# Optimization experiments

Measured on AMD Instinct MI355X. Metric: run time of the kernel, lower is better.

## Reference

```python
import jax, jax.numpy as jnp
import numpy as np

N_NODES = 100000


def gcn_conv(x, src, dst, norm, W, b, n):
    # x: [N, F_in]; src/dst: [E'] (with self loops); norm: [E']
    xw = x @ W                                   # [N, F_out]
    msg = xw[src] * norm[:, None]                # [E', F_out]
    agg = jax.ops.segment_sum(msg, dst, num_segments=n)
    return agg + b


def _self_loops_and_norm(edge_index, n):
    loop = jnp.arange(n, dtype=edge_index.dtype)
    src = jnp.concatenate([edge_index[0], loop])
    dst = jnp.concatenate([edge_index[1], loop])
    deg = jax.ops.segment_sum(jnp.ones_like(dst, dtype=jnp.float32), dst, num_segments=n)
    dis = jnp.where(deg > 0, jax.lax.rsqrt(jnp.maximum(deg, 1.0)), 0.0)
    norm = dis[src] * dis[dst]
    return src, dst, norm


def setup_inputs() -> dict:
    key = jax.random.key(0)
    k1, k2, k3, k4, k5, k6 = jax.random.split(key, 6)
    n, e = N_NODES, 1600000
    f_in, f_hid, f_out = 64, 128, 64
    x = jax.random.normal(k1, (n, f_in), dtype=jnp.float32)
    edge_index = jax.random.randint(k2, (2, e), 0, n, dtype=jnp.int64)
    # Glorot init like PyG GCNConv
    W0 = jax.random.normal(k3, (f_in, f_hid), dtype=jnp.float32) * (1.0 / np.sqrt(f_in))
    b0 = jnp.zeros((f_hid,), dtype=jnp.float32)
    W1 = jax.random.normal(k4, (f_hid, f_out), dtype=jnp.float32) * (1.0 / np.sqrt(f_hid))
    b1 = jnp.zeros((f_out,), dtype=jnp.float32)
    return {"x": x, "edge_index": edge_index, "W0": W0, "b0": b0, "W1": W1, "b1": b1}


def reference(x, edge_index, W0, b0, W1, b1):
    n = x.shape[0]
    src, dst, norm = _self_loops_and_norm(edge_index, n)
    h = gcn_conv(x, src, dst, norm, W0, b0, n)
    h = jax.nn.relu(h)
    out = gcn_conv(h, src, dst, norm, W1, b1, n)
    return jax.nn.sigmoid(out)
```

## Files before the change

kernel.cpp:

```cpp
#include <hip/hip_runtime.h>
#include <hip/hip_fp16.h>
#include <math.h>


#define FIN 64
#define FHID 128
#define FOUT 64
#define NPB 128
#define LOGNPB 7
#define BMAX 800
#define G 256
#define CAP 4096

typedef _Float16 f16x2 __attribute__((ext_vector_type(2)));

#if defined(__has_builtin)
#if __has_builtin(__builtin_amdgcn_fdot2)
#define HAS_FDOT2 1
#endif
#endif

__device__ __forceinline__ float dot2(f16x2 a, f16x2 b, float c) {
#ifdef HAS_FDOT2
    return __builtin_amdgcn_fdot2(a, b, c, false);
#else
    c = fmaf((float)a[0], (float)b[0], c);
    return fmaf((float)a[1], (float)b[1], c);
#endif
}


__global__ __launch_bounds__(1024) void khist(const int* __restrict__ dst,
                                              int* __restrict__ ghist,
                                              int e, int B, int chunk) {
    __shared__ int h[BMAX];
    int g = blockIdx.x, t = threadIdx.x;
    for (int i = t; i < B; i += 1024) h[i] = 0;
    __syncthreads();
    int lo = g * chunk, hi = min(e, lo + chunk);
    for (int i = lo + t; i < hi; i += 1024)
        atomicAdd(&h[dst[i] >> LOGNPB], 1);
    __syncthreads();
    for (int i = t; i < B; i += 1024) ghist[i * G + g] = h[i];
}

__global__ __launch_bounds__(256) void kscanA(const int* __restrict__ ghist,
                                              int* __restrict__ gbase,
                                              int* __restrict__ tot, int B) {
    int b = blockIdx.x * 256 + threadIdx.x;
    if (b >= B) return;
    int run = 0;
    #pragma unroll 8
    for (int g = 0; g < G; ++g) {
        int v = ghist[b * G + g];
        gbase[b * G + g] = run;
        run += v;
    }
    tot[b] = run;
}

__global__ __launch_bounds__(256) void kscanB(const int* __restrict__ tot,
                                              int* __restrict__ bb, int B, int e) {
    __shared__ int s[256];
    __shared__ int chunkoff;
    int t = threadIdx.x;
    if (t == 0) chunkoff = 0;
    __syncthreads();
    for (int c0 = 0; c0 < B; c0 += 256) {
        int v = (c0 + t < B) ? tot[c0 + t] : 0;
        s[t] = v;
        __syncthreads();
        for (int off = 1; off < 256; off <<= 1) {
            int u = (t >= off) ? s[t - off] : 0;
            __syncthreads();
            s[t] += u;
            __syncthreads();
        }
        if (c0 + t < B) bb[c0 + t] = s[t] - v + chunkoff;
        __syncthreads();
        if (t == 255) chunkoff += s[255];
        __syncthreads();
    }
    if (t == 0) bb[B] = e;
}

__global__ __launch_bounds__(1024) void kscatter(const int* __restrict__ src,
                                                 const int* __restrict__ dst,
                                                 const int* __restrict__ gbase,
                                                 const int* __restrict__ bb,
                                                 unsigned* __restrict__ pk,
                                                 int e, int B, int chunk) {
    __shared__ int cur[BMAX];
    int g = blockIdx.x, t = threadIdx.x;
    for (int b = t; b < B; b += 1024) cur[b] = bb[b] + gbase[b * G + g];
    __syncthreads();
    int lo = g * chunk, hi = min(e, lo + chunk);
    for (int i = lo + t; i < hi; i += 1024) {
        int d = dst[i], s = src[i], b = d >> LOGNPB;
        int p = atomicAdd(&cur[b], 1);
        pk[p] = ((unsigned)(d & (NPB - 1)) << 17) | (unsigned)s;
    }
}

__global__ __launch_bounds__(256) void kpsort(const unsigned* __restrict__ pk,
                                              const int* __restrict__ bb,
                                              const float* __restrict__ x,
                                              int* __restrict__ ssrc,
                                              int* __restrict__ rp,
                                              float* __restrict__ dis,
                                              __half* __restrict__ yh,
                                              int n, int e) {
    __shared__ int cnt[NPB];
    __shared__ int pre[NPB];
    __shared__ float disl[NPB];
    __shared__ unsigned stage[CAP];
    int b = blockIdx.x, t = threadIdx.x;
    int lo = bb[b], hi = bb[b + 1], m = hi - lo;
    if (t < NPB) cnt[t] = 0;
    __syncthreads();
    for (int i = lo + t; i < hi; i += 256)
        atomicAdd(&cnt[pk[i] >> 17], 1);
    __syncthreads();
    if (t < NPB) pre[t] = cnt[t];
    __syncthreads();
    #pragma unroll
    for (int off = 1; off < NPB; off <<= 1) {
        int v = (t < NPB && t >= off) ? pre[t - off] : 0;
        __syncthreads();
        if (t < NPB) pre[t] += v;
        __syncthreads();
    }
    if (t < NPB) {
        int node = b * NPB + t;
        int c = cnt[t];
        int bs = lo + pre[t] - c;
        float dv = rsqrtf(1.0f + (float)c);
        disl[t] = dv;
        if (node < n) {
            rp[node] = bs;
            dis[node] = dv;
        }
        cnt[t] = bs - lo;
    }
    if (b == 0 && t == 0) rp[n] = e;
    __syncthreads();
    if (m <= CAP) {
        for (int i = lo + t; i < hi; i += 256) {
            unsigned v = pk[i];
            int p = atomicAdd(&cnt[v >> 17], 1);
            stage[p] = v & 0x1FFFF;
        }
        __syncthreads();
        for (int i = t; i < m; i += 256) ssrc[lo + i] = (int)stage[i];
    } else {
        for (int i = lo + t; i < hi; i += 256) {
            unsigned v = pk[i];
            int p = atomicAdd(&cnt[v >> 17], 1);
            ssrc[lo + p] = (int)(v & 0x1FFFF);
        }
    }
    for (int i = t; i < NPB * 16; i += 256) {
        int node = b * NPB + (i >> 4);
        if (node < n) {
            float d = disl[i >> 4];
            int gi = b * (NPB * 16) + i;
            float4 v = reinterpret_cast<const float4*>(x)[gi];
            __half2 h0, h1;
            h0.x = __float2half(d * v.x); h0.y = __float2half(d * v.y);
            h1.x = __float2half(d * v.z); h1.y = __float2half(d * v.w);
            reinterpret_cast<__half2*>(yh)[gi * 2 + 0] = h0;
            reinterpret_cast<__half2*>(yh)[gi * 2 + 1] = h1;
        }
    }
}

__global__ __launch_bounds__(256) void k_pull16(
        const int* __restrict__ rp, const int* __restrict__ ssrc,
        const float* __restrict__ dis, const __half* __restrict__ yh,
        const float* __restrict__ b1, float* __restrict__ outp,
        __half* __restrict__ outph, int n, int sig) {
    int node4 = blockIdx.x * 4 + (threadIdx.x >> 6);
    if (node4 >= n) return;
    int node = __builtin_amdgcn_readfirstlane(node4);
    int f = threadIdx.x & 63;
    float a0 = __half2float(yh[(size_t)node * 64 + f]);
    float a1 = 0.f, a2 = 0.f, a3 = 0.f, a4 = 0.f, a5 = 0.f, a6 = 0.f, a7 = 0.f;
    int j = rp[node], end = rp[node + 1];
    for (; j + 7 < end; j += 8) {
        int s0 = ssrc[j],     s1 = ssrc[j + 1], s2 = ssrc[j + 2], s3 = ssrc[j + 3];
        int s4 = ssrc[j + 4], s5 = ssrc[j + 5], s6 = ssrc[j + 6], s7 = ssrc[j + 7];
        a0 += __half2float(yh[(size_t)s0 * 64 + f]);
        a1 += __half2float(yh[(size_t)s1 * 64 + f]);
        a2 += __half2float(yh[(size_t)s2 * 64 + f]);
        a3 += __half2float(yh[(size_t)s3 * 64 + f]);
        a4 += __half2float(yh[(size_t)s4 * 64 + f]);
        a5 += __half2float(yh[(size_t)s5 * 64 + f]);
        a6 += __half2float(yh[(size_t)s6 * 64 + f]);
        a7 += __half2float(yh[(size_t)s7 * 64 + f]);
    }
    for (; j + 1 < end; j += 2) {
        int s0 = ssrc[j], s1 = ssrc[j + 1];
        a0 += __half2float(yh[(size_t)s0 * 64 + f]);
        a1 += __half2float(yh[(size_t)s1 * 64 + f]);
    }
    if (j < end)
        a0 += __half2float(yh[(size_t)ssrc[j] * 64 + f]);
    float v = dis[node] * (((a0 + a1) + (a2 + a3)) + ((a4 + a5) + (a6 + a7)));
    if (sig) {
        v += b1[f];
        outp[(size_t)node * 64 + f] = 1.0f / (1.0f + expf(-v));
    } else {
        outph[(size_t)node * 64 + f] = __float2half(v);
    }
}

__global__ __launch_bounds__(256) void k_gemm1(
        const __half* __restrict__ in,
        const float* __restrict__ W0,
        const float* __restrict__ b0,
        __half* __restrict__ h,
        int n, int nwaves) {
    int gw = blockIdx.x * 4 + (threadIdx.x >> 6);
    int lane = threadIdx.x & 63;

    f16x2 w0a[32], w0b[32];
    #pragma unroll
    for (int i = 0; i < 32; ++i) {
        w0a[i] = (f16x2){(_Float16)W0[(2 * i) * FHID + lane],
                         (_Float16)W0[(2 * i + 1) * FHID + lane]};
        w0b[i] = (f16x2){(_Float16)W0[(2 * i) * FHID + 64 + lane],
                         (_Float16)W0[(2 * i + 1) * FHID + 64 + lane]};
    }
    float ba = b0[lane], bbias = b0[64 + lane];

    for (int task = gw; task < n; task += nwaves) {
        int row = __builtin_amdgcn_readfirstlane(task);
        const f16x2* srow = reinterpret_cast<const f16x2*>(in + (size_t)row * FIN);
        float aa = ba, ab = bbias;
        #pragma unroll
        for (int i = 0; i < 32; ++i) {
            f16x2 xv = srow[i];
            aa = dot2(xv, w0a[i], aa);
            ab = dot2(xv, w0b[i], ab);
        }
        h[(size_t)row * FHID + lane]      = __float2half(fmaxf(aa, 0.0f));
        h[(size_t)row * FHID + 64 + lane] = __float2half(fmaxf(ab, 0.0f));
    }
}

__global__ __launch_bounds__(256) void k_gemm2(
        const __half* __restrict__ h,
        const float* __restrict__ W1,
        const float* __restrict__ dis,
        __half* __restrict__ yh,
        int n, int nwaves) {
    int gw = blockIdx.x * 4 + (threadIdx.x >> 6);
    int lane = threadIdx.x & 63;

    f16x2 w1c[64];
    #pragma unroll
    for (int i = 0; i < 64; ++i)
        w1c[i] = (f16x2){(_Float16)W1[(2 * i) * FOUT + lane],
                         (_Float16)W1[(2 * i + 1) * FOUT + lane]};

    for (int task = gw; task < n; task += nwaves) {
        int row = __builtin_amdgcn_readfirstlane(task);
        const f16x2* hrow = reinterpret_cast<const f16x2*>(h + (size_t)row * FHID);
        float acc = 0.0f;
        #pragma unroll
        for (int i = 0; i < 64; ++i)
            acc = dot2(hrow[i], w1c[i], acc);
        yh[(size_t)row * FOUT + lane] = __float2half(dis[row] * acc);
    }
}

extern "C" void kernel_launch(void* const* d_in, const int* in_sizes, int n_in,
                              void* d_out, int out_size, void* d_ws, size_t ws_size,
                              hipStream_t stream) {
    const float* x   = (const float*)d_in[0];
    const int*   ei  = (const int*)d_in[1];
    const float* W0  = (const float*)d_in[2];
    const float* b0  = (const float*)d_in[3];
    const float* W1  = (const float*)d_in[4];
    const float* b1  = (const float*)d_in[5];
    float*       out = (float*)d_out;

    const int n = in_sizes[0] / FIN;
    const int e = in_sizes[1] / 2;
    const int* src = ei;
    const int* dst = ei + e;
    if (n > (1 << 17)) return;

    const int B = (n + NPB - 1) / NPB;
    if (B > BMAX) return;
    const int chunk = (e + G - 1) / G;

    float*    dis  = (float*)d_ws;
    __half*   bufh = (__half*)(dis + n);
    int*      ssrc = (int*)(bufh + (size_t)n * FIN);
    int*      rp   = ssrc + e;
    __half*   yh   = (__half*)(rp + (n + 1));
    char*     region = (char*)(yh + (size_t)n * FIN);
    __half*   hh   = (__half*)region;
    unsigned* pk   = (unsigned*)region;
    int*      ghist = (int*)(pk + e);
    int*      gbase = ghist + (size_t)B * G;
    int*      tot   = gbase + (size_t)B * G;
    int*      bb    = tot + B;
    size_t region_sz = (size_t)n * FHID * sizeof(__half);
    {
        size_t pkchain = (size_t)((char*)(bb + B + 1) - region);
        if (pkchain > region_sz) region_sz = pkchain;
    }
    size_t need = (size_t)(region - (char*)d_ws) + region_sz;
    if (ws_size < need) return;

    khist<<<G, 1024, 0, stream>>>(dst, ghist, e, B, chunk);
    kscanA<<<(B + 255) / 256, 256, 0, stream>>>(ghist, gbase, tot, B);
    kscanB<<<1, 256, 0, stream>>>(tot, bb, B, e);
    kscatter<<<G, 1024, 0, stream>>>(src, dst, gbase, bb, pk, e, B, chunk);
    kpsort<<<B, 256, 0, stream>>>(pk, bb, x, ssrc, rp, dis, yh, n, e);

    k_pull16<<<(n + 3) / 4, 256, 0, stream>>>(rp, ssrc, dis, yh, b1,
                                              (float*)nullptr, bufh, n, 0);

    const int blocks = 2048, nwaves = blocks * 4;
    k_gemm1<<<blocks, 256, 0, stream>>>(bufh, W0, b0, hh, n, nwaves);
    k_gemm2<<<blocks, 256, 0, stream>>>(hh, W1, dis, yh, n, nwaves);

    k_pull16<<<(n + 3) / 4, 256, 0, stream>>>(rp, ssrc, dis, yh, b1,
                                              out, (__half*)nullptr, n, 1);
}
```

Measured before the change: 239.4 us.

## Fuse CSR build kernels into one persistent kernel with software grid barriers

Replaces the five CSR-construction kernels (histogram, two scans, scatter, per-bucket sort) with one persistent 256-block kernel that separates the phases with atomic grid barriers. The per-bucket prefix scan now uses wave shuffles instead of a serial loop per thread. The aim is to remove kernel-launch gaps and the tiny single-block scan launches. In exchange, the per-bucket sort now runs on only 256 blocks looping over about 782 buckets, which lowers parallelism in that phase. It also assumes all 256 blocks are co-resident, since the spin barrier deadlocks otherwise.

```diff
diff --git a/kernel.cpp b/kernel.cpp
--- a/kernel.cpp
+++ b/kernel.cpp
@@ -10,6 +10,7 @@
 #define LOGNPB 7
 #define BMAX 800
 #define G 256
+#define TPB 1024
 #define CAP 4096
 
 typedef _Float16 f16x2 __attribute__((ext_vector_type(2)));
@@ -29,147 +30,161 @@
 #endif
 }
 
-
-__global__ __launch_bounds__(1024) void khist(const int* __restrict__ dst,
-                                              int* __restrict__ ghist,
-                                              int e, int B, int chunk) {
+__device__ __forceinline__ void gridbar(int* cnt, int* gen, int nb) {
+    __syncthreads();
+    if (threadIdx.x == 0) {
+        int g = __hip_atomic_load(gen, __ATOMIC_ACQUIRE, __HIP_MEMORY_SCOPE_AGENT);
+        int prev = __hip_atomic_fetch_add(cnt, 1, __ATOMIC_ACQ_REL,
+                                          __HIP_MEMORY_SCOPE_AGENT);
+        if (prev == nb - 1) {
+            __hip_atomic_store(cnt, 0, __ATOMIC_RELAXED, __HIP_MEMORY_SCOPE_AGENT);
+            __hip_atomic_fetch_add(gen, 1, __ATOMIC_ACQ_REL,
+                                   __HIP_MEMORY_SCOPE_AGENT);
+        } else {
+            while (__hip_atomic_load(gen, __ATOMIC_ACQUIRE,
+                                     __HIP_MEMORY_SCOPE_AGENT) == g)
+                __builtin_amdgcn_s_sleep(1);
+        }
+    }
+    __syncthreads();
+}
+
+__global__ __launch_bounds__(TPB, 1) void kbuild(
+        const int* __restrict__ src, const int* __restrict__ dst,
+        const float* __restrict__ x,
+        int* __restrict__ ghist, int* __restrict__ gbase,
+        int* __restrict__ tot, int* __restrict__ bb,
+        unsigned* __restrict__ pk, int* __restrict__ ssrc,
+        int* __restrict__ rp, float* __restrict__ dis,
+        __half* __restrict__ yh, int* bar,
+        int n, int e, int B, int chunk) {
     __shared__ int h[BMAX];
-    int g = blockIdx.x, t = threadIdx.x;
-    for (int i = t; i < B; i += 1024) h[i] = 0;
-    __syncthreads();
-    int lo = g * chunk, hi = min(e, lo + chunk);
-    for (int i = lo + t; i < hi; i += 1024)
-        atomicAdd(&h[dst[i] >> LOGNPB], 1);
-    __syncthreads();
-    for (int i = t; i < B; i += 1024) ghist[i * G + g] = h[i];
-}
-
-__global__ __launch_bounds__(256) void kscanA(const int* __restrict__ ghist,
-                                              int* __restrict__ gbase,
-                                              int* __restrict__ tot, int B) {
-    int b = blockIdx.x * 256 + threadIdx.x;
-    if (b >= B) return;
-    int run = 0;
-    #pragma unroll 8
-    for (int g = 0; g < G; ++g) {
-        int v = ghist[b * G + g];
-        gbase[b * G + g] = run;
-        run += v;
-    }
-    tot[b] = run;
-}
-
-__global__ __launch_bounds__(256) void kscanB(const int* __restrict__ tot,
-                                              int* __restrict__ bb, int B, int e) {
-    __shared__ int s[256];
-    __shared__ int chunkoff;
-    int t = threadIdx.x;
-    if (t == 0) chunkoff = 0;
-    __syncthreads();
-    for (int c0 = 0; c0 < B; c0 += 256) {
-        int v = (c0 + t < B) ? tot[c0 + t] : 0;
-        s[t] = v;
-        __syncthreads();
-        for (int off = 1; off < 256; off <<= 1) {
-            int u = (t >= off) ? s[t - off] : 0;
-            __syncthreads();
-            s[t] += u;
-            __syncthreads();
-        }
-        if (c0 + t < B) bb[c0 + t] = s[t] - v + chunkoff;
-        __syncthreads();
-        if (t == 255) chunkoff += s[255];
-        __syncthreads();
-    }
-    if (t == 0) bb[B] = e;
-}
-
-__global__ __launch_bounds__(1024) void kscatter(const int* __restrict__ src,
-                                                 const int* __restrict__ dst,
-                                                 const int* __restrict__ gbase,
-                                                 const int* __restrict__ bb,
-                                                 unsigned* __restrict__ pk,
-                                                 int e, int B, int chunk) {
-    __shared__ int cur[BMAX];
-    int g = blockIdx.x, t = threadIdx.x;
-    for (int b = t; b < B; b += 1024) cur[b] = bb[b] + gbase[b * G + g];
-    __syncthreads();
-    int lo = g * chunk, hi = min(e, lo + chunk);
-    for (int i = lo + t; i < hi; i += 1024) {
-        int d = dst[i], s = src[i], b = d >> LOGNPB;
-        int p = atomicAdd(&cur[b], 1);
-        pk[p] = ((unsigned)(d & (NPB - 1)) << 17) | (unsigned)s;
-    }
-}
-
-__global__ __launch_bounds__(256) void kpsort(const unsigned* __restrict__ pk,
-                                              const int* __restrict__ bb,
-                                              const float* __restrict__ x,
-                                              int* __restrict__ ssrc,
-                                              int* __restrict__ rp,
-                                              float* __restrict__ dis,
-                                              __half* __restrict__ yh,
-                                              int n, int e) {
-    __shared__ int cnt[NPB];
-    __shared__ int pre[NPB];
+    __shared__ int cnt[NPB], pre[NPB];
     __shared__ float disl[NPB];
     __shared__ unsigned stage[CAP];
-    int b = blockIdx.x, t = threadIdx.x;
-    int lo = bb[b], hi = bb[b + 1], m = hi - lo;
-    if (t < NPB) cnt[t] = 0;
-    __syncthreads();
-    for (int i = lo + t; i < hi; i += 256)
-        atomicAdd(&cnt[pk[i] >> 17], 1);
-    __syncthreads();
-    if (t < NPB) pre[t] = cnt[t];
-    __syncthreads();
-    #pragma unroll
-    for (int off = 1; off < NPB; off <<= 1) {
-        int v = (t < NPB && t >= off) ? pre[t - off] : 0;
-        __syncthreads();
-        if (t < NPB) pre[t] += v;
-        __syncthreads();
-    }
-    if (t < NPB) {
-        int node = b * NPB + t;
-        int c = cnt[t];
-        int bs = lo + pre[t] - c;
-        float dv = rsqrtf(1.0f + (float)c);
-        disl[t] = dv;
-        if (node < n) {
-            rp[node] = bs;
-            dis[node] = dv;
-        }
-        cnt[t] = bs - lo;
-    }
-    if (b == 0 && t == 0) rp[n] = e;
-    __syncthreads();
-    if (m <= CAP) {
-        for (int i = lo + t; i < hi; i += 256) {
-            unsigned v = pk[i];
-            int p = atomicAdd(&cnt[v >> 17], 1);
-            stage[p] = v & 0x1FFFF;
-        }
-        __syncthreads();
-        for (int i = t; i < m; i += 256) ssrc[lo + i] = (int)stage[i];
-    } else {
-        for (int i = lo + t; i < hi; i += 256) {
-            unsigned v = pk[i];
-            int p = atomicAdd(&cnt[v >> 17], 1);
-            ssrc[lo + p] = (int)(v & 0x1FFFF);
-        }
-    }
-    for (int i = t; i < NPB * 16; i += 256) {
-        int node = b * NPB + (i >> 4);
-        if (node < n) {
-            float d = disl[i >> 4];
-            int gi = b * (NPB * 16) + i;
-            float4 v = reinterpret_cast<const float4*>(x)[gi];
-            __half2 h0, h1;
-            h0.x = __float2half(d * v.x); h0.y = __float2half(d * v.y);
-            h1.x = __float2half(d * v.z); h1.y = __float2half(d * v.w);
-            reinterpret_cast<__half2*>(yh)[gi * 2 + 0] = h0;
-            reinterpret_cast<__half2*>(yh)[gi * 2 + 1] = h1;
+    __shared__ int sscan[TPB];
+
+    int g = blockIdx.x, t = threadIdx.x;
+    int lo = g * chunk, hi = min(e, lo + chunk);
+
+    for (int i = t; i < B; i += TPB) h[i] = 0;
+    __syncthreads();
+    for (int i = lo + t; i < hi; i += TPB)
+        atomicAdd(&h[dst[i] >> LOGNPB], 1);
+    __syncthreads();
+    for (int i = t; i < B; i += TPB) ghist[i * G + g] = h[i];
+
+    gridbar(bar, bar + 1, G);
+
+    {
+        int wid = g * (TPB / 64) + (t >> 6);
+        int lane = t & 63;
+        if (wid < B) {
+            int base = wid * G + lane * 4;
+            int v0 = ghist[base + 0], v1 = ghist[base + 1];
+            int v2 = ghist[base + 2], v3 = ghist[base + 3];
+            int s4 = v0 + v1 + v2 + v3;
+            int sc = s4;
+            #pragma unroll
+            for (int off = 1; off < 64; off <<= 1) {
+                int u = __shfl_up(sc, off);
+                if (lane >= off) sc += u;
+            }
+            int run = sc - s4;
+            gbase[base + 0] = run; run += v0;
+            gbase[base + 1] = run; run += v1;
+            gbase[base + 2] = run; run += v2;
+            gbase[base + 3] = run;
+            if (lane == 63) tot[wid] = sc;
+        }
+    }
+
+    gridbar(bar, bar + 1, G);
+
+    if (g == 0) {
+        int v = (t < B) ? tot[t] : 0;
+        sscan[t] = v;
+        __syncthreads();
+        for (int off = 1; off < TPB; off <<= 1) {
+            int u = (t >= off) ? sscan[t - off] : 0;
+            __syncthreads();
+            sscan[t] += u;
+            __syncthreads();
+        }
+        if (t < B) bb[t] = sscan[t] - v;
+        if (t == 0) bb[B] = e;
+    }
+
+    gridbar(bar, bar + 1, G);
+
+    for (int b = t; b < B; b += TPB) h[b] = bb[b] + gbase[b * G + g];
+    __syncthreads();
+    for (int i = lo + t; i < hi; i += TPB) {
+        int d = dst[i], s = src[i], b = d >> LOGNPB;
+        int p = atomicAdd(&h[b], 1);
+        pk[p] = ((unsigned)(d & (NPB - 1)) << 17) | (unsigned)s;
+    }
+
+    gridbar(bar, bar + 1, G);
+
+    for (int b = g; b < B; b += G) {
+        __syncthreads();
+        int blo = bb[b], bhi = bb[b + 1], m = bhi - blo;
+        if (t < NPB) cnt[t] = 0;
+        __syncthreads();
+        for (int i = blo + t; i < bhi; i += TPB)
+            atomicAdd(&cnt[pk[i] >> 17], 1);
+        __syncthreads();
+        if (t < NPB) pre[t] = cnt[t];
+        __syncthreads();
+        #pragma unroll
+        for (int off = 1; off < NPB; off <<= 1) {
+            int v = (t < NPB && t >= off) ? pre[t - off] : 0;
+            __syncthreads();
+            if (t < NPB) pre[t] += v;
+            __syncthreads();
+        }
+        if (t < NPB) {
+            int node = b * NPB + t;
+            int c = cnt[t];
+            int bs = blo + pre[t] - c;
+            float dv = rsqrtf(1.0f + (float)c);
+            disl[t] = dv;
+            if (node < n) {
+                rp[node] = bs;
+                dis[node] = dv;
+            }
+            cnt[t] = bs - blo;
+        }
+        if (b == 0 && t == 0) rp[n] = e;
+        __syncthreads();
+        if (m <= CAP) {
+            for (int i = blo + t; i < bhi; i += TPB) {
+                unsigned v = pk[i];
+                int p = atomicAdd(&cnt[v >> 17], 1);
+                stage[p] = v & 0x1FFFF;
+            }
+            __syncthreads();
+            for (int i = t; i < m; i += TPB) ssrc[blo + i] = (int)stage[i];
+        } else {
+            for (int i = blo + t; i < bhi; i += TPB) {
+                unsigned v = pk[i];
+                int p = atomicAdd(&cnt[v >> 17], 1);
+                ssrc[blo + p] = (int)(v & 0x1FFFF);
+            }
+        }
+        for (int i = t; i < NPB * 16; i += TPB) {
+            int node = b * NPB + (i >> 4);
+            if (node < n) {
+                float d = disl[i >> 4];
+                int gi = b * (NPB * 16) + i;
+                float4 v = reinterpret_cast<const float4*>(x)[gi];
+                __half2 h0, h1;
+                h0.x = __float2half(d * v.x); h0.y = __float2half(d * v.y);
+                h1.x = __float2half(d * v.z); h1.y = __float2half(d * v.w);
+                reinterpret_cast<__half2*>(yh)[gi * 2 + 0] = h0;
+                reinterpret_cast<__half2*>(yh)[gi * 2 + 1] = h1;
+            }
         }
     }
 }
@@ -307,19 +322,19 @@
     int*      gbase = ghist + (size_t)B * G;
     int*      tot   = gbase + (size_t)B * G;
     int*      bb    = tot + B;
+    int*      bar   = bb + (B + 1);
     size_t region_sz = (size_t)n * FHID * sizeof(__half);
     {
-        size_t pkchain = (size_t)((char*)(bb + B + 1) - region);
+        size_t pkchain = (size_t)((char*)(bar + 2) - region);
         if (pkchain > region_sz) region_sz = pkchain;
     }
     size_t need = (size_t)(region - (char*)d_ws) + region_sz;
     if (ws_size < need) return;
 
-    khist<<<G, 1024, 0, stream>>>(dst, ghist, e, B, chunk);
-    kscanA<<<(B + 255) / 256, 256, 0, stream>>>(ghist, gbase, tot, B);
-    kscanB<<<1, 256, 0, stream>>>(tot, bb, B, e);
-    kscatter<<<G, 1024, 0, stream>>>(src, dst, gbase, bb, pk, e, B, chunk);
-    kpsort<<<B, 256, 0, stream>>>(pk, bb, x, ssrc, rp, dis, yh, n, e);
+    hipMemsetAsync(bar, 0, 2 * sizeof(int), stream);
+
+    kbuild<<<G, TPB, 0, stream>>>(src, dst, x, ghist, gbase, tot, bb,
+                                  pk, ssrc, rp, dis, yh, bar, n, e, B, chunk);
 
     k_pull16<<<(n + 3) / 4, 256, 0, stream>>>(rp, ssrc, dis, yh, b1,
                                               (float*)nullptr, bufh, n, 0);
```

After: 342.0 us. 42.9% more time.
